# Kernel tuning notes

Measured on AMD Instinct MI355X. Metric: run time of the kernel, lower is better.

The kernel has to match this reference:

```python
import jax, jax.numpy as jnp
import numpy as np

B, C, M = 2048, 1, 80  # M = max_object; matrices are (M+1)x(M+1)


def setup_inputs() -> dict:
    key = jax.random.key(0)
    k1, k2, k3, k4 = jax.random.split(key, 4)
    inp = {
        "input": jax.random.normal(k1, (B, C, M + 1, M + 1), dtype=jnp.float32),
        "target": jax.random.randint(k2, (B, C, M + 1, M + 1), 0, 2, dtype=jnp.int32),
        "mask0": jax.random.randint(k3, (B, C, M + 1), 0, 2, dtype=jnp.int32),
        "mask1": jax.random.randint(k4, (B, C, M + 1), 0, 2, dtype=jnp.int32),
        "outputs": 0,
        "current_fair_labels": 0,
        "next_fair_labels": 0,
    }
    return inp


def reference(input, target, mask0, mask1, outputs, current_fair_labels, next_fair_labels):
    f32 = jnp.float32
    m0 = mask0.astype(f32)[:, :, :, None]   # [B,C,M+1,1] (row mask, broadcast over cols)
    m1 = mask1.astype(f32)[:, :, None, :]   # [B,C,1,M+1] (col mask, broadcast over rows)
    mask_region = m0 * m1                    # [B,C,M+1,M+1]
    mask_region_pre = mask_region.at[:, :, M, :].set(0.0)   # zero last row
    mask_region_next = mask_region.at[:, :, :, M].set(0.0)  # zero last col
    mask_region_union = mask_region_pre * mask_region_next

    input_pre = jax.nn.softmax(mask_region_pre * input, axis=3)
    input_next = jax.nn.softmax(mask_region_next * input, axis=2)
    input_all = input_pre.at[:, :, :M, :M].set(
        jnp.maximum(input_pre, input_next)[:, :, :M, :M])

    t = target.astype(jnp.bool_).astype(f32)
    target_pre = mask_region_pre * t
    target_next = mask_region_next * t
    target_union = mask_region_union * t

    target_num = t.sum()
    n_pre = target_pre.sum()
    n_next = target_next.sum()
    n_union = target_union.sum()

    s_pre = -(target_pre * jnp.log(input_pre)).sum()
    loss_pre = jnp.where(n_pre > 0, s_pre / n_pre, s_pre)

    s_next = -(target_next * jnp.log(input_next)).sum()
    loss_next = jnp.where(n_next > 0, s_next / n_next, s_next)

    s_all = -(target_pre * jnp.log(input_all)).sum()
    loss = jnp.where((n_pre > 0) & (n_next > 0), s_all / n_pre, s_all)

    # |1 - p_pre - (1 - p_next)| == |p_next - p_pre|
    s_sim = (target_union * jnp.abs(input_next - input_pre)).sum()
    loss_similarity = jnp.where(n_union > 0, s_sim / target_num, s_sim)

    # accuracy on "pre" direction (argmax over cols, drop last row)
    idx_t_pre = jnp.argmax(target_pre, axis=3)[:, :, :-1]
    indexes_pre = jnp.argmax(input_all, axis=3)[:, :, :-1]
    mpre = mask0.astype(f32)[:, :, :-1]
    n_mpre = mpre.sum()
    s_acc_pre = ((indexes_pre == idx_t_pre).astype(f32) * mpre).sum()
    accuracy_pre = jnp.where(n_mpre > 0, s_acc_pre / n_mpre, s_acc_pre + 1.0)

    # accuracy on "next" direction (argmax over rows, drop last col)
    idx_t_next = jnp.argmax(target_next, axis=2)[:, :, :-1]
    indexes_next = jnp.argmax(input_next, axis=2)[:, :, :-1]
    mnext = mask1.astype(f32)[:, :, :-1]
    n_mnext = mnext.sum()
    s_acc_next = ((indexes_next == idx_t_next).astype(f32) * mnext).sum()
    accuracy_next = jnp.where(n_mnext > 0, s_acc_next / n_mnext, s_acc_next + 1.0)

    total = (loss_pre + loss_next + loss + loss_similarity) / 4.0
    return (loss_pre, loss_next, loss_similarity, total,
            accuracy_pre, accuracy_next, (accuracy_pre + accuracy_next) / 2.0,
            indexes_pre)
```

## Files before the change

### kernel.cpp

```cpp
#include <hip/hip_runtime.h>

#define M1 81
#define MSZ 80
#define NEL (M1 * M1)
#define NTW ((NEL + 31) / 32)
#define NACC 12
#define BIGKC 1.0e30f


__global__ __launch_bounds__(512, 8) void sst_main(
    const float* __restrict__ input,
    const int* __restrict__ target,
    const int* __restrict__ mask0,
    const int* __restrict__ mask1,
    float* __restrict__ out_idx,
    float* __restrict__ part,
    int slices)
{
    __shared__ __align__(16) float s_x[NEL];
    __shared__ unsigned s_tb[NTW];
    __shared__ float s_m0[M1], s_m1[M1];
    __shared__ float s_kc[M1];
    __shared__ float s_invc[M1];
    __shared__ float s_pA[486];
    __shared__ float s_pC[480];
    __shared__ float s_pV[486];
    __shared__ unsigned char s_pI[486];
    __shared__ unsigned char s_pT[486];
    __shared__ unsigned char s_ci[MSZ];
    __shared__ int s_ct[MSZ];
    __shared__ unsigned s_m1w[4];
    __shared__ float s_wv[8][NACC];

    const int tid   = threadIdx.x;
    const int lane  = tid & 63;
    const int w     = tid >> 6;
    const int slice = blockIdx.x;
    const size_t base = (size_t)slice * NEL;

    if (tid < M1) s_m0[tid] = (float)mask0[slice * M1 + tid];
    else if (tid >= 128 && tid < 128 + M1) s_m1[tid - 128] = (float)mask1[slice * M1 + (tid - 128)];
    if (tid >= 256 && tid < 256 + MSZ) s_ct[tid - 256] = 0x7fffffff;

    float a[NACC];
#pragma unroll
    for (int k = 0; k < NACC; ++k) a[k] = 0.0f;

    __syncthreads();

    const bool actA = (tid < 486);
    const int cA = tid / 6, jA = tid - 6 * (tid / 6);
    const int r0 = jA * 13 + ((jA < 3) ? jA : 3);
    const bool has14 = (jA < 3);
    float v[14];
    if (actA) {
        const float* gp = input + base + (size_t)r0 * M1 + cA;
#pragma unroll
        for (int i = 0; i < 13; ++i) v[i] = gp[i * M1];
        v[13] = gp[((jA < 5) ? 13 : 0) * M1];
    }

    int tpre[13];
#pragma unroll
    for (int k = 0; k < 13; ++k) {
        const int i = tid + (k << 9);
        tpre[k] = (i < NEL) ? target[base + i] : 0;
    }

    if (w == 0) {
        const unsigned long long m = __ballot(s_m1[lane] != 0.0f);
        if (lane == 0) { s_m1w[0] = (unsigned)m; s_m1w[1] = (unsigned)(m >> 32); }
    } else if (w == 1) {
        float vv = 0.0f;
        if (lane < 17) vv = s_m1[64 + lane];
        const unsigned long long m = __ballot(vv != 0.0f);
        if (lane == 0) { s_m1w[2] = (unsigned)m; s_m1w[3] = 0u; }
    }

    if (actA) {
        const float m1c = s_m1[cA];
        float cs = 0.0f, bv = -1.0f;
        int bi = r0;
        int idx = r0 * M1 + cA;
#pragma unroll
        for (int i = 0; i < 13; ++i, idx += M1) {
            const int r = r0 + i;
            const float z = m1c * s_m0[r] * v[i];
            const float e = __expf(z);
            s_x[idx] = e;
            cs += e;
            if (e > bv) { bv = e; bi = r; }
        }
        if (has14) {
            const int r = r0 + 13;
            const float z = m1c * s_m0[r] * v[13];
            const float e = __expf(z);
            s_x[idx] = e;
            cs += e;
            if (e > bv) { bv = e; bi = r; }
        }
        s_pA[tid] = cs; s_pV[tid] = bv; s_pI[tid] = (unsigned char)bi;
    }

#pragma unroll
    for (int k = 0; k < 13; ++k) {
        const int i = tid + (k << 9);
        if (i < NEL) {
            const unsigned long long m = __ballot(tpre[k] != 0);
            if (lane == 0) {
                a[0] += (float)__popcll(m);
                const int w2 = (i >> 5) & ~1;
                s_tb[w2] = (unsigned)m;
                if (w2 + 1 < NTW) s_tb[w2 + 1] = (unsigned)(m >> 32);
            }
        }
    }
    __syncthreads();

    if (tid < 480) {
        const int r = tid / 6, j = tid - 6 * (tid / 6);
        const int c0 = j * 13 + ((j < 3) ? j : 3);
        const int len = (j < 3) ? 14 : 13;
        const int rb = r * M1 + c0;
        float rs = 0.0f;
        for (int i = 0; i < len; ++i) rs += s_x[rb + i];
        s_pC[tid] = rs;
    } else {
        const int u = tid - 480;
        for (int c = u; c < M1; c += 32) {
            if (c < MSZ) {
                const int b = 6 * c;
                float cs = 0.0f;
#pragma unroll
                for (int k = 0; k < 6; ++k) cs += s_pA[b + k];
                float bv = s_pV[b]; int bi = s_pI[b];
#pragma unroll
                for (int k = 1; k < 6; ++k) {
                    const float vv = s_pV[b + k];
                    if (vv > bv) { bv = vv; bi = s_pI[b + k]; }
                }
                s_kc[c] = __logf(cs);
                s_invc[c] = 1.0f / cs;
                s_ci[c] = (unsigned char)bi;
            } else {
                s_kc[c] = BIGKC;
                s_invc[c] = 0.0f;
            }
        }
    }
    __syncthreads();

    if (tid < 480) {
        const int r = tid / 6, j = tid - 6 * (tid / 6);
        const int c0 = j * 13 + ((j < 3) ? j : 3);
        const int len = (j < 3) ? 14 : 13;
        const int rb = r * M1;
        const int pb = 6 * r;
        const float rs = s_pC[pb] + s_pC[pb + 1] + s_pC[pb + 2]
                       + s_pC[pb + 3] + s_pC[pb + 4] + s_pC[pb + 5];
        const float lr = __logf(rs), invr = 1.0f / rs;
        const float m0f = s_m0[r];

        const int bp = rb + c0;
        const unsigned long long tw64 =
            ((unsigned long long)s_tb[(bp >> 5) + 1] << 32) | s_tb[bp >> 5];
        const int mp0 = c0 >> 5;
        const unsigned long long mw64 =
            ((unsigned long long)s_m1w[mp0 + 1] << 32) | s_m1w[mp0];
        const unsigned lenmask = (1u << len) - 1u;
        unsigned wb = (unsigned)(tw64 >> (bp & 31)) & (unsigned)(mw64 >> (c0 & 31)) & lenmask;
        if (m0f == 0.0f) wb = 0u;

        const unsigned w3 = (j == 5) ? (wb & 0x0FFFu) : wb;
        a[1] += (float)__popc(wb);
        a[2] += (float)__popc(w3);
        a[3] += (float)__popc(w3);
        const int ti = wb ? (c0 + __ffs(wb) - 1) : 127;

        float bv = -1.0f; int bi = c0;
        for (int i = 0; i < len; ++i) {
            const int c = c0 + i;
            const float val = s_x[rb + c] * fmaxf(invr, s_invc[c]);
            if (val > bv) { bv = val; bi = c; }
        }
        unsigned wl = wb;
        while (wl) {
            const int b = __ffs(wl) - 1; wl &= wl - 1u;
            const int c = c0 + b;
            const float e = s_x[rb + c];
            const float z = __logf(e);
            a[4] += lr - z;
            a[6] += fminf(lr, s_kc[c]) - z;
            if (c != MSZ) {
                a[5] += s_kc[c] - z;
                a[7] = fmaf(e, fabsf(s_invc[c] - invr), a[7]);
                atomicMin(&s_ct[c], r);
            }
        }
        s_pV[tid] = bv; s_pI[tid] = (unsigned char)bi; s_pT[tid] = (unsigned char)ti;
    } else if (tid < 486) {
        const int j = tid - 480;
        const int c0 = j * 13 + ((j < 3) ? j : 3);
        const int len = (j < 3) ? 14 : 13;
        const int rb = MSZ * M1;
        const float m80 = s_m0[MSZ];
        const int bp = rb + c0;
        const unsigned long long tw64 =
            ((unsigned long long)s_tb[(bp >> 5) + 1] << 32) | s_tb[bp >> 5];
        const int mp0 = c0 >> 5;
        const unsigned long long mw64 =
            ((unsigned long long)s_m1w[mp0 + 1] << 32) | s_m1w[mp0];
        const unsigned lenmask = (1u << len) - 1u;
        unsigned wb = (unsigned)(tw64 >> (bp & 31)) & (unsigned)(mw64 >> (c0 & 31)) & lenmask;
        if (m80 == 0.0f) wb = 0u;
        if (j == 5) wb &= 0x0FFFu;
        a[2] += (float)__popc(wb);
        while (wb) {
            const int b = __ffs(wb) - 1; wb &= wb - 1u;
            const int c = c0 + b;
            a[5] += s_kc[c] - __logf(s_x[rb + c]);
            atomicMin(&s_ct[c], MSZ);
        }
    }
    __syncthreads();

    if (tid < MSZ) {
        const int b = 6 * tid;
        float bv = s_pV[b]; int bi = s_pI[b];
#pragma unroll
        for (int k = 1; k < 6; ++k) {
            const float vv = s_pV[b + k];
            if (vv > bv) { bv = vv; bi = s_pI[b + k]; }
        }
        int ti = 127;
#pragma unroll
        for (int k = 0; k < 6; ++k) ti = min(ti, (int)s_pT[b + k]);
        if (ti == 127) ti = 0;
        out_idx[(size_t)slice * MSZ + tid] = (float)bi;
        const float m0f = s_m0[tid];
        a[8]  += (bi == ti) ? m0f : 0.0f;
        a[10] += m0f;
    } else if (tid >= 128 && tid < 128 + MSZ) {
        const int c = tid - 128;
        const int ctv = s_ct[c];
        const int ti = (ctv == 0x7fffffff) ? 0 : ctv;
        const int bi = (int)s_ci[c];
        const float m1c = s_m1[c];
        a[9]  += (bi == ti) ? m1c : 0.0f;
        a[11] += m1c;
    }

#pragma unroll
    for (int k = 0; k < NACC; ++k) {
        float vv = a[k];
        for (int off = 32; off > 0; off >>= 1) vv += __shfl_down(vv, off);
        if (lane == 0) s_wv[w][k] = vv;
    }
    __syncthreads();
    if (tid < NACC) {
        float s = 0.0f;
#pragma unroll
        for (int ww = 0; ww < 8; ++ww) s += s_wv[ww][tid];
        part[(size_t)tid * slices + slice] = s;
    }
}

__global__ __launch_bounds__(256) void sst_final(
    const float* __restrict__ part, int slices, float* __restrict__ out)
{
    __shared__ double s_part[4][NACC];
    const int tid = threadIdx.x;
    double l[NACC];
#pragma unroll
    for (int k = 0; k < NACC; ++k) l[k] = 0.0;
    for (int s = tid; s < slices; s += 256) {
#pragma unroll
        for (int k = 0; k < NACC; ++k) l[k] += (double)part[(size_t)k * slices + s];
    }
#pragma unroll
    for (int k = 0; k < NACC; ++k) {
        double v = l[k];
        for (int off = 32; off > 0; off >>= 1) v += __shfl_down(v, off);
        if ((tid & 63) == 0) s_part[tid >> 6][k] = v;
    }
    __syncthreads();
    if (tid == 0) {
        double g[NACC];
#pragma unroll
        for (int k = 0; k < NACC; ++k)
            g[k] = s_part[0][k] + s_part[1][k] + s_part[2][k] + s_part[3][k];
        const double tnum = g[0], npre = g[1], nnext = g[2], nunion = g[3];
        const double spre = g[4], snext = g[5], sall = g[6], ssim = g[7];
        const double accp = g[8], accn = g[9], nmp = g[10], nmn = g[11];
        const double loss_pre  = (npre > 0.0) ? spre / npre : spre;
        const double loss_next = (nnext > 0.0) ? snext / nnext : snext;
        const double loss      = (npre > 0.0 && nnext > 0.0) ? sall / npre : sall;
        const double loss_sim  = (nunion > 0.0) ? ssim / tnum : ssim;
        const double total = (loss_pre + loss_next + loss + loss_sim) * 0.25;
        const double ap = (nmp > 0.0) ? accp / nmp : accp + 1.0;
        const double an = (nmn > 0.0) ? accn / nmn : accn + 1.0;
        out[0] = (float)loss_pre;
        out[1] = (float)loss_next;
        out[2] = (float)loss_sim;
        out[3] = (float)total;
        out[4] = (float)ap;
        out[5] = (float)an;
        out[6] = (float)((ap + an) * 0.5);
    }
}

extern "C" void kernel_launch(void* const* d_in, const int* in_sizes, int n_in,
                              void* d_out, int out_size, void* d_ws, size_t ws_size,
                              hipStream_t stream) {
    const float* input  = (const float*)d_in[0];
    const int*   target = (const int*)d_in[1];
    const int*   mask0  = (const int*)d_in[2];
    const int*   mask1  = (const int*)d_in[3];
    float* out = (float*)d_out;
    float* part = (float*)d_ws;

    const int slices = in_sizes[0] / NEL;

    sst_main<<<slices, 512, 0, stream>>>(input, target, mask0, mask1, out + 7, part, slices);
    sst_final<<<1, 256, 0, stream>>>(part, slices, out);
}
```

Measured before the change: 155.6 us.

## Repartition per-row/column work to 4 lanes with shuffle reductions, drop barriers

Work is reassigned from 6 threads per column or row to 4 adjacent lanes per column or row (324 active threads), so partial sums and argmax are combined with wave shuffles instead of shared-memory partial arrays. This removes one block-wide barrier and the separate phases that combined column and row partials. The final 12-accumulator reduction now writes every thread's values into the reused s_x buffer and sums them with 96 threads plus shuffles, replacing the per-warp shuffle-down tree. Each thread does more serial work (20 elements instead of 13) and fewer threads are active, which trades parallelism for fewer synchronisations and less shared-memory traffic.

```diff
diff --git a/kernel.cpp b/kernel.cpp
--- a/kernel.cpp
+++ b/kernel.cpp
@@ -6,6 +6,7 @@
 #define NTW ((NEL + 31) / 32)
 #define NACC 12
 #define BIGKC 1.0e30f
+#define REDP 517
 
 
 __global__ __launch_bounds__(512, 8) void sst_main(
@@ -22,21 +23,20 @@
     __shared__ float s_m0[M1], s_m1[M1];
     __shared__ float s_kc[M1];
     __shared__ float s_invc[M1];
-    __shared__ float s_pA[486];
-    __shared__ float s_pC[480];
-    __shared__ float s_pV[486];
-    __shared__ unsigned char s_pI[486];
-    __shared__ unsigned char s_pT[486];
-    __shared__ unsigned char s_ci[MSZ];
+    __shared__ unsigned char s_ci[M1];
     __shared__ int s_ct[MSZ];
     __shared__ unsigned s_m1w[4];
-    __shared__ float s_wv[8][NACC];
 
     const int tid   = threadIdx.x;
     const int lane  = tid & 63;
-    const int w     = tid >> 6;
     const int slice = blockIdx.x;
     const size_t base = (size_t)slice * NEL;
+
+    const bool act = (tid < 4 * M1);
+    const int g   = tid >> 2;
+    const int j4  = tid & 3;
+    const int c0j = (j4 == 0) ? 0 : (1 + 20 * j4);
+    const int lm1 = (j4 == 0) ? 0x1FFFFF : 0xFFFFF;
 
     if (tid < M1) s_m0[tid] = (float)mask0[slice * M1 + tid];
     else if (tid >= 128 && tid < 128 + M1) s_m1[tid - 128] = (float)mask1[slice * M1 + (tid - 128)];
@@ -48,16 +48,12 @@
 
     __syncthreads();
 
-    const bool actA = (tid < 486);
-    const int cA = tid / 6, jA = tid - 6 * (tid / 6);
-    const int r0 = jA * 13 + ((jA < 3) ? jA : 3);
-    const bool has14 = (jA < 3);
-    float v[14];
-    if (actA) {
-        const float* gp = input + base + (size_t)r0 * M1 + cA;
-#pragma unroll
-        for (int i = 0; i < 13; ++i) v[i] = gp[i * M1];
-        v[13] = gp[((jA < 5) ? 13 : 0) * M1];
+    float v[21];
+    if (act) {
+        const float* gp = input + base + (size_t)c0j * M1 + g;
+#pragma unroll
+        for (int i = 0; i < 20; ++i) v[i] = gp[i * M1];
+        v[20] = gp[((j4 == 0) ? 20 : 0) * M1];
     }
 
     int tpre[13];
@@ -67,39 +63,52 @@
         tpre[k] = (i < NEL) ? target[base + i] : 0;
     }
 
-    if (w == 0) {
+    if ((tid >> 6) == 0) {
         const unsigned long long m = __ballot(s_m1[lane] != 0.0f);
         if (lane == 0) { s_m1w[0] = (unsigned)m; s_m1w[1] = (unsigned)(m >> 32); }
-    } else if (w == 1) {
+    } else if ((tid >> 6) == 1) {
         float vv = 0.0f;
         if (lane < 17) vv = s_m1[64 + lane];
         const unsigned long long m = __ballot(vv != 0.0f);
         if (lane == 0) { s_m1w[2] = (unsigned)m; s_m1w[3] = 0u; }
     }
 
-    if (actA) {
-        const float m1c = s_m1[cA];
+    if (act) {
+        const int c = g;
+        const float m1c = s_m1[c];
         float cs = 0.0f, bv = -1.0f;
-        int bi = r0;
-        int idx = r0 * M1 + cA;
-#pragma unroll
-        for (int i = 0; i < 13; ++i, idx += M1) {
-            const int r = r0 + i;
+        int bi = c0j;
+        int idx = c0j * M1 + c;
+#pragma unroll
+        for (int i = 0; i < 20; ++i, idx += M1) {
+            const int r = c0j + i;
             const float z = m1c * s_m0[r] * v[i];
             const float e = __expf(z);
             s_x[idx] = e;
             cs += e;
             if (e > bv) { bv = e; bi = r; }
         }
-        if (has14) {
-            const int r = r0 + 13;
-            const float z = m1c * s_m0[r] * v[13];
+        if (j4 == 0) {
+            const float z = m1c * s_m0[20] * v[20];
             const float e = __expf(z);
-            s_x[idx] = e;
+            s_x[20 * M1 + c] = e;
             cs += e;
-            if (e > bv) { bv = e; bi = r; }
-        }
-        s_pA[tid] = cs; s_pV[tid] = bv; s_pI[tid] = (unsigned char)bi;
+            if (e > bv) { bv = e; bi = 20; }
+        }
+#pragma unroll
+        for (int m = 1; m <= 2; m <<= 1) {
+            const float pcs = __shfl_xor(cs, m);
+            const float pbv = __shfl_xor(bv, m);
+            const int   pbi = __shfl_xor(bi, m);
+            cs += pcs;
+            const bool take = (lane & m) ? (pbv >= bv) : (pbv > bv);
+            if (take) { bv = pbv; bi = pbi; }
+        }
+        if (j4 == 0) {
+            s_kc[c]   = (c == MSZ) ? BIGKC : __logf(cs);
+            s_invc[c] = (c == MSZ) ? 0.0f  : 1.0f / cs;
+            s_ci[c]   = (unsigned char)bi;
+        }
     }
 
 #pragma unroll
@@ -117,151 +126,111 @@
     }
     __syncthreads();
 
-    if (tid < 480) {
-        const int r = tid / 6, j = tid - 6 * (tid / 6);
-        const int c0 = j * 13 + ((j < 3) ? j : 3);
-        const int len = (j < 3) ? 14 : 13;
-        const int rb = r * M1 + c0;
-        float rs = 0.0f;
-        for (int i = 0; i < len; ++i) rs += s_x[rb + i];
-        s_pC[tid] = rs;
-    } else {
-        const int u = tid - 480;
-        for (int c = u; c < M1; c += 32) {
-            if (c < MSZ) {
-                const int b = 6 * c;
-                float cs = 0.0f;
-#pragma unroll
-                for (int k = 0; k < 6; ++k) cs += s_pA[b + k];
-                float bv = s_pV[b]; int bi = s_pI[b];
-#pragma unroll
-                for (int k = 1; k < 6; ++k) {
-                    const float vv = s_pV[b + k];
-                    if (vv > bv) { bv = vv; bi = s_pI[b + k]; }
-                }
-                s_kc[c] = __logf(cs);
-                s_invc[c] = 1.0f / cs;
-                s_ci[c] = (unsigned char)bi;
-            } else {
-                s_kc[c] = BIGKC;
-                s_invc[c] = 0.0f;
-            }
-        }
-    }
-    __syncthreads();
-
-    if (tid < 480) {
-        const int r = tid / 6, j = tid - 6 * (tid / 6);
-        const int c0 = j * 13 + ((j < 3) ? j : 3);
-        const int len = (j < 3) ? 14 : 13;
+    if (act) {
+        const int r = g;
         const int rb = r * M1;
-        const int pb = 6 * r;
-        const float rs = s_pC[pb] + s_pC[pb + 1] + s_pC[pb + 2]
-                       + s_pC[pb + 3] + s_pC[pb + 4] + s_pC[pb + 5];
-        const float lr = __logf(rs), invr = 1.0f / rs;
-        const float m0f = s_m0[r];
-
-        const int bp = rb + c0;
+        const int bp = rb + c0j;
         const unsigned long long tw64 =
             ((unsigned long long)s_tb[(bp >> 5) + 1] << 32) | s_tb[bp >> 5];
-        const int mp0 = c0 >> 5;
+        const int mp0 = c0j >> 5;
         const unsigned long long mw64 =
             ((unsigned long long)s_m1w[mp0 + 1] << 32) | s_m1w[mp0];
-        const unsigned lenmask = (1u << len) - 1u;
-        unsigned wb = (unsigned)(tw64 >> (bp & 31)) & (unsigned)(mw64 >> (c0 & 31)) & lenmask;
-        if (m0f == 0.0f) wb = 0u;
-
-        const unsigned w3 = (j == 5) ? (wb & 0x0FFFu) : wb;
-        a[1] += (float)__popc(wb);
-        a[2] += (float)__popc(w3);
-        a[3] += (float)__popc(w3);
-        const int ti = wb ? (c0 + __ffs(wb) - 1) : 127;
-
-        float bv = -1.0f; int bi = c0;
-        for (int i = 0; i < len; ++i) {
-            const int c = c0 + i;
-            const float val = s_x[rb + c] * fmaxf(invr, s_invc[c]);
-            if (val > bv) { bv = val; bi = c; }
-        }
-        unsigned wl = wb;
-        while (wl) {
-            const int b = __ffs(wl) - 1; wl &= wl - 1u;
-            const int c = c0 + b;
-            const float e = s_x[rb + c];
-            const float z = __logf(e);
-            a[4] += lr - z;
-            a[6] += fminf(lr, s_kc[c]) - z;
-            if (c != MSZ) {
-                a[5] += s_kc[c] - z;
-                a[7] = fmaf(e, fabsf(s_invc[c] - invr), a[7]);
-                atomicMin(&s_ct[c], r);
-            }
-        }
-        s_pV[tid] = bv; s_pI[tid] = (unsigned char)bi; s_pT[tid] = (unsigned char)ti;
-    } else if (tid < 486) {
-        const int j = tid - 480;
-        const int c0 = j * 13 + ((j < 3) ? j : 3);
-        const int len = (j < 3) ? 14 : 13;
-        const int rb = MSZ * M1;
-        const float m80 = s_m0[MSZ];
-        const int bp = rb + c0;
-        const unsigned long long tw64 =
-            ((unsigned long long)s_tb[(bp >> 5) + 1] << 32) | s_tb[bp >> 5];
-        const int mp0 = c0 >> 5;
-        const unsigned long long mw64 =
-            ((unsigned long long)s_m1w[mp0 + 1] << 32) | s_m1w[mp0];
-        const unsigned lenmask = (1u << len) - 1u;
-        unsigned wb = (unsigned)(tw64 >> (bp & 31)) & (unsigned)(mw64 >> (c0 & 31)) & lenmask;
-        if (m80 == 0.0f) wb = 0u;
-        if (j == 5) wb &= 0x0FFFu;
-        a[2] += (float)__popc(wb);
-        while (wb) {
-            const int b = __ffs(wb) - 1; wb &= wb - 1u;
-            const int c = c0 + b;
-            a[5] += s_kc[c] - __logf(s_x[rb + c]);
-            atomicMin(&s_ct[c], MSZ);
+        unsigned wb = (unsigned)(tw64 >> (bp & 31)) & (unsigned)(mw64 >> (c0j & 31)) & (unsigned)lm1;
+
+        if (r < MSZ) {
+            const float m0f = s_m0[r];
+            if (m0f == 0.0f) wb = 0u;
+            float rs = 0.0f;
+#pragma unroll
+            for (int i = 0; i < 20; ++i) rs += s_x[rb + c0j + i];
+            if (j4 == 0) rs += s_x[rb + 20];
+            rs += __shfl_xor(rs, 1);
+            rs += __shfl_xor(rs, 2);
+            const float lr = __logf(rs), invr = 1.0f / rs;
+
+            const unsigned w3 = (j4 == 3) ? (wb & 0x7FFFFu) : wb;
+            a[1] += (float)__popc(wb);
+            a[2] += (float)__popc(w3);
+            a[3] += (float)__popc(w3);
+            int ti = wb ? (c0j + __ffs(wb) - 1) : 127;
+
+            float bv = -1.0f; int bi = c0j;
+#pragma unroll
+            for (int i = 0; i < 20; ++i) {
+                const int c = c0j + i;
+                const float val = s_x[rb + c] * fmaxf(invr, s_invc[c]);
+                if (val > bv) { bv = val; bi = c; }
+            }
+            if (j4 == 0) {
+                const float val = s_x[rb + 20] * fmaxf(invr, s_invc[20]);
+                if (val > bv) { bv = val; bi = 20; }
+            }
+            unsigned wl = wb;
+            while (wl) {
+                const int b = __ffs(wl) - 1; wl &= wl - 1u;
+                const int c = c0j + b;
+                const float e = s_x[rb + c];
+                const float z = __logf(e);
+                a[4] += lr - z;
+                a[6] += fminf(lr, s_kc[c]) - z;
+                if (c != MSZ) {
+                    a[5] += s_kc[c] - z;
+                    a[7] = fmaf(e, fabsf(s_invc[c] - invr), a[7]);
+                    atomicMin(&s_ct[c], r);
+                }
+            }
+#pragma unroll
+            for (int m = 1; m <= 2; m <<= 1) {
+                const float pbv = __shfl_xor(bv, m);
+                const int   pbi = __shfl_xor(bi, m);
+                const int   pti = __shfl_xor(ti, m);
+                const bool take = (lane & m) ? (pbv >= bv) : (pbv > bv);
+                if (take) { bv = pbv; bi = pbi; }
+                ti = min(ti, pti);
+            }
+            if (j4 == 0) {
+                if (ti == 127) ti = 0;
+                out_idx[(size_t)slice * MSZ + r] = (float)bi;
+                a[8]  += (bi == ti) ? m0f : 0.0f;
+                a[10] += m0f;
+            }
+        } else {
+            if (s_m0[MSZ] == 0.0f) wb = 0u;
+            if (j4 == 3) wb &= 0x7FFFFu;
+            a[2] += (float)__popc(wb);
+            while (wb) {
+                const int b = __ffs(wb) - 1; wb &= wb - 1u;
+                const int c = c0j + b;
+                a[5] += s_kc[c] - __logf(s_x[rb + c]);
+                atomicMin(&s_ct[c], MSZ);
+            }
         }
     }
     __syncthreads();
 
     if (tid < MSZ) {
-        const int b = 6 * tid;
-        float bv = s_pV[b]; int bi = s_pI[b];
-#pragma unroll
-        for (int k = 1; k < 6; ++k) {
-            const float vv = s_pV[b + k];
-            if (vv > bv) { bv = vv; bi = s_pI[b + k]; }
-        }
-        int ti = 127;
-#pragma unroll
-        for (int k = 0; k < 6; ++k) ti = min(ti, (int)s_pT[b + k]);
-        if (ti == 127) ti = 0;
-        out_idx[(size_t)slice * MSZ + tid] = (float)bi;
-        const float m0f = s_m0[tid];
-        a[8]  += (bi == ti) ? m0f : 0.0f;
-        a[10] += m0f;
-    } else if (tid >= 128 && tid < 128 + MSZ) {
-        const int c = tid - 128;
-        const int ctv = s_ct[c];
+        const int ctv = s_ct[tid];
         const int ti = (ctv == 0x7fffffff) ? 0 : ctv;
-        const int bi = (int)s_ci[c];
-        const float m1c = s_m1[c];
+        const int bi = (int)s_ci[tid];
+        const float m1c = s_m1[tid];
         a[9]  += (bi == ti) ? m1c : 0.0f;
         a[11] += m1c;
     }
 
-#pragma unroll
-    for (int k = 0; k < NACC; ++k) {
-        float vv = a[k];
-        for (int off = 32; off > 0; off >>= 1) vv += __shfl_down(vv, off);
-        if (lane == 0) s_wv[w][k] = vv;
-    }
-    __syncthreads();
-    if (tid < NACC) {
+    float* red = s_x;
+#pragma unroll
+    for (int k = 0; k < NACC; ++k) red[k * REDP + tid] = a[k];
+    __syncthreads();
+    if (tid < 96) {
+        const int k = tid >> 3, u = tid & 7;
+        const int b0 = k * REDP + u * 64;
+        const int i0 = u * 4;
         float s = 0.0f;
-#pragma unroll
-        for (int ww = 0; ww < 8; ++ww) s += s_wv[ww][tid];
-        part[(size_t)tid * slices + slice] = s;
+        for (int i = 0; i < 64; ++i) s += red[b0 + ((i0 + i) & 63)];
+        s += __shfl_xor(s, 1);
+        s += __shfl_xor(s, 2);
+        s += __shfl_xor(s, 4);
+        if (u == 0) part[(size_t)k * slices + slice] = s;
     }
 }
 
```

After: 151.7 us. -2.5%, faster.
